# Performance work log

Measured on AMD Instinct MI355X. Metric: run time of the kernel, lower is better.

The kernel has to match this reference:

```python
import jax, jax.numpy as jnp
import numpy as np

N = 20000      # nodes
E = 256000     # edges
H = 8          # heads
DIN = 256      # in_dim_struct / in_dim_semantic
DH = 32        # num_hidden per head (H*DH == DIN for GT residual)
PRED = 32      # pred_dim (relation embedding dim)
REL = 16       # rel_num
NEG = 0.2      # negative_slope for GAT attention
ALPHA = 0.5    # args.fusion
NUM_LAYERS = 2


def seg_softmax(e, seg, n):
    # softmax over edges grouped by destination node; e: [E, ...], seg: [E]
    m = jax.ops.segment_max(e, seg, num_segments=n)
    ex = jnp.exp(e - m[seg])
    s = jax.ops.segment_sum(ex, seg, num_segments=n)
    return ex / (s[seg] + 1e-9)


def setup_inputs() -> dict:
    key = jax.random.key(0)
    ks = jax.random.split(key, 24)
    f32 = jnp.float32
    def rn(k, shape, scale=0.05):
        return jax.random.normal(k, shape, dtype=f32) * scale
    return {
        "feats_struct": jax.random.normal(ks[0], (N, DIN), f32),
        "feats_semantic": jax.random.normal(ks[1], (N, DIN), f32),
        "centrality": jax.random.uniform(ks[2], (N,), f32),
        # fused per-head scoring MLP (heads[0] small Sequentials batched over H)
        "Ws1": rn(ks[3], (H, DIN, DIN // 2)),
        "bs1": jnp.zeros((H, DIN // 2), f32),
        "Ws2": rn(ks[4], (H, DIN // 2)),
        "bs2": jnp.zeros((H,), f32),
        "rel_emb": rn(ks[5], (REL, PRED), 1.0),
        # SALayer params (2 layers, per-head scalar channels)
        "sa_w": rn(ks[6], (NUM_LAYERS, H), 1.0),
        "sa_al": rn(ks[7], (NUM_LAYERS, H), 1.0),
        "sa_ar": rn(ks[8], (NUM_LAYERS, H), 1.0),
        "sa_We": rn(ks[9], (NUM_LAYERS, PRED, H)),
        # GTLayer params
        "Wq": rn(ks[10], (DIN, H * DH)),
        "bq": jnp.zeros((H * DH,), f32),
        "Wk": rn(ks[11], (DIN, H * DH)),
        "bk": jnp.zeros((H * DH,), f32),
        "Wv": rn(ks[12], (DIN, H * DH)),
        "bv": jnp.zeros((H * DH,), f32),
        "We_gt": rn(ks[13], (PRED, H * DH)),
        "bn_gamma": jnp.ones((H * DH,), f32),
        "bn_beta": jnp.zeros((H * DH,), f32),
        "Wout": rn(ks[14], (H * DH, 1)),
        "bout": jnp.zeros((1,), f32),
        # centrality scale params
        "gamma": jnp.ones((1, H), f32),
        "beta": jnp.zeros((1, H), f32),
        "edge_types": jax.random.randint(ks[15], (E,), 0, REL),
        "edge_src": jax.random.randint(ks[16], (E,), 0, N),
        "edge_dst": jax.random.randint(ks[17], (E,), 0, N),
    }


def _forward(feats_struct, feats_semantic, centrality, Ws1, bs1, Ws2, bs2,
             rel_emb, sa_w, sa_al, sa_ar, sa_We, Wq, bq, Wk, bk, Wv, bv,
             We_gt, bn_gamma, bn_beta, Wout, bout, gamma, beta,
             edge_types, edge_src, edge_dst):
    n = feats_struct.shape[0]
    edge_feats = rel_emb[edge_types]                                   # [E, PRED]

    # ---- structural channel: fused per-head scoring MLPs ----
    h1 = jax.nn.relu(jnp.einsum('nd,hdk->nhk', feats_struct, Ws1) + bs1)  # [N,H,DIN/2]
    h = jnp.einsum('nhk,hk->nh', h1, Ws2) + bs2                           # [N,H]

    # ---- SALayer stack (GAT-style, per-head scalar features) ----
    for l in range(NUM_LAYERS):
        z = h * sa_w[l]                                                 # [N,H]
        e = jax.nn.leaky_relu(z[edge_src] * sa_al[l] + z[edge_dst] * sa_ar[l]
                              + edge_feats @ sa_We[l], NEG)             # [E,H]
        attn = seg_softmax(e, edge_dst, n)                              # [E,H]
        out = jax.ops.segment_sum(attn * z[edge_src], edge_dst, num_segments=n)
        h = jax.nn.elu(out + z)                                         # residual + activation
        if l != NUM_LAYERS - 1:
            h = jnp.mean(h, axis=-1, keepdims=True)
            h = jnp.tile(h, (1, H))
    logits_struct = h                                                   # [N,H]

    # ---- semantic channel: Graph Transformer layer (edge_mode='MUL') ----
    q = (feats_semantic @ Wq + bq).reshape(n, H, DH)
    k = (feats_semantic @ Wk + bk).reshape(n, H, DH)
    v = (feats_semantic @ Wv + bv).reshape(n, H, DH)
    ep = (edge_feats @ We_gt).reshape(-1, H, DH)                        # [E,H,DH]
    ke = k[edge_src] * ep                                               # MUL edge gating
    score = jnp.sum(q[edge_dst] * ke, axis=-1) / jnp.sqrt(jnp.float32(DH))  # [E,H]
    attn = seg_softmax(score, edge_dst, n)                              # [E,H]
    agg = jax.ops.segment_sum(attn[..., None] * v[edge_src], edge_dst,
                              num_segments=n).reshape(n, H * DH)
    agg = agg + feats_semantic                                          # residual (H*DH == DIN)
    mu = jnp.mean(agg, axis=0)
    var = jnp.var(agg, axis=0)
    agg = (agg - mu) / jnp.sqrt(var + 1e-5) * bn_gamma + bn_beta        # batch norm
    h_sem = jax.nn.relu(agg)
    logits_semantic = h_sem @ Wout + bout                               # [N,1]

    # ---- fusion + centrality gamma/beta scaling ----
    logits = ALPHA * logits_struct + (1.0 - ALPHA) * logits_semantic    # [N,H]
    scaled = (centrality[:, None] * gamma + beta) * logits              # [N,H]
    return jax.nn.leaky_relu(jnp.mean(scaled, axis=-1, keepdims=True), 0.01)


def reference(feats_struct, feats_semantic, centrality, Ws1, bs1, Ws2, bs2,
              rel_emb, sa_w, sa_al, sa_ar, sa_We, Wq, bq, Wk, bk, Wv, bv,
              We_gt, bn_gamma, bn_beta, Wout, bout, gamma, beta,
              edge_types, edge_src, edge_dst):
    return _forward(feats_struct, feats_semantic, centrality, Ws1, bs1, Ws2, bs2,
                    rel_emb, sa_w, sa_al, sa_ar, sa_We, Wq, bq, Wk, bk, Wv, bv,
                    We_gt, bn_gamma, bn_beta, Wout, bout, gamma, beta,
                    edge_types, edge_src, edge_dst)
```

## Files before the change

kernel.cpp:

```cpp
#include <hip/hip_runtime.h>
#include <hip/hip_bf16.h>
#include <math.h>

#define N_NODES 20000
#define N_EDGES 256000

typedef __attribute__((ext_vector_type(8))) __bf16 bf16x8;
typedef __attribute__((ext_vector_type(8))) unsigned short u16x8;
typedef __attribute__((ext_vector_type(4))) float f32x4;

static __device__ __forceinline__ unsigned short f2bf(float f) {
  unsigned u = __float_as_uint(f);
  unsigned r = (u + 0x7fffu + ((u >> 16) & 1u)) >> 16;
  return (unsigned short)r;
}
static __device__ __forceinline__ float b2f(unsigned short u) {
  return __uint_as_float((unsigned)u << 16);
}


__global__ void k_tables(const float* __restrict__ rel_emb,
                         const float* __restrict__ sa_We,
                         const float* __restrict__ We_gt,
                         float* __restrict__ saTab, float* __restrict__ epTab) {
  int t = threadIdx.x;
  {
    int l = t >> 7, r = (t >> 3) & 15, h = t & 7;
    float acc = 0.f;
    for (int p = 0; p < 32; ++p)
      acc += rel_emb[r * 32 + p] * sa_We[l * 256 + p * 8 + h];
    saTab[t] = acc;
  }
  for (int r = 0; r < 16; ++r) {
    float acc = 0.f;
    for (int p = 0; p < 32; ++p)
      acc += rel_emb[r * 32 + p] * We_gt[p * 256 + t];
    epTab[r * 256 + t] = acc;
  }
}

__global__ void k_hist(const int* __restrict__ e_dst, int* __restrict__ deg) {
  int e = blockIdx.x * 256 + threadIdx.x;
  if (e < N_EDGES) atomicAdd(&deg[e_dst[e]], 1);
}

__global__ void k_scan(const int* __restrict__ deg, int* __restrict__ rowPtr,
                       int* __restrict__ cursor) {
  const int CH = (N_NODES + 255) / 256;
  int t = threadIdx.x;
  int b0 = t * CH, b1 = min(b0 + CH, N_NODES);
  int s = 0;
  for (int i = b0; i < b1; ++i) s += deg[i];
  __shared__ int part[256];
  part[t] = s;
  __syncthreads();
  for (int off = 1; off < 256; off <<= 1) {
    int add = (t >= off) ? part[t - off] : 0;
    __syncthreads();
    part[t] += add;
    __syncthreads();
  }
  int run = (t == 0) ? 0 : part[t - 1];
  for (int i = b0; i < b1; ++i) {
    rowPtr[i] = run;
    cursor[i] = run;
    run += deg[i];
  }
  if (t == 0) rowPtr[N_NODES] = part[255];
}

__global__ void k_fill(const int* __restrict__ e_dst, const int* __restrict__ e_src,
                       const int* __restrict__ e_type, int* __restrict__ cursor,
                       int* __restrict__ csrSrc, int* __restrict__ csrType) {
  int e = blockIdx.x * 256 + threadIdx.x;
  if (e >= N_EDGES) return;
  int d = e_dst[e];
  int pos = atomicAdd(&cursor[d], 1);
  csrSrc[pos] = e_src[e];
  csrType[pos] = e_type[e];
}


__global__ void k_convX(const float* __restrict__ Xs, const float* __restrict__ Xm,
                        ushort* __restrict__ Xsb, ushort* __restrict__ Xmb) {
  size_t i = ((size_t)blockIdx.x * 256 + threadIdx.x) * 4;
  float4 a = *(const float4*)(Xs + i);
  ushort4 ua = {f2bf(a.x), f2bf(a.y), f2bf(a.z), f2bf(a.w)};
  *(ushort4*)(Xsb + i) = ua;
  float4 b = *(const float4*)(Xm + i);
  ushort4 ub = {f2bf(b.x), f2bf(b.y), f2bf(b.z), f2bf(b.w)};
  *(ushort4*)(Xmb + i) = ub;
}

__global__ void k_tws1(const float* __restrict__ Ws1, ushort* __restrict__ Ws1t) {
  int h = blockIdx.x >> 7, kcol = blockIdx.x & 127, d = threadIdx.x;
  Ws1t[((size_t)h * 128 + kcol) * 256 + d] = f2bf(Ws1[((size_t)h * 256 + d) * 128 + kcol]);
}

__global__ void k_twqkv(const float* __restrict__ Wq, const float* __restrict__ Wk,
                        const float* __restrict__ Wv, ushort* __restrict__ Wt) {
  int m = blockIdx.x >> 8, n = blockIdx.x & 255, d = threadIdx.x;
  const float* W = (m == 0) ? Wq : (m == 1) ? Wk : Wv;
  Wt[((size_t)m * 256 + n) * 256 + d] = f2bf(W[(size_t)d * 256 + n]);
}


__global__ __launch_bounds__(256) void k_mlp_mfma(
    const ushort* __restrict__ Xb, const ushort* __restrict__ Ws1t,
    const float* __restrict__ bs1, const float* __restrict__ Ws2,
    const float* __restrict__ bs2, float* __restrict__ h0) {
  __shared__ ushort Ab[64][136];
  __shared__ ushort Bb[128][136];
  int tid = threadIdx.x;
  int h = blockIdx.y;
  int base = blockIdx.x * 64;
  int wv = tid >> 6, lane = tid & 63;
  int l15 = lane & 15, lhi = lane >> 4;
  f32x4 acc[8];
  #pragma unroll
  for (int nt = 0; nt < 8; ++nt) acc[nt] = (f32x4){0.f, 0.f, 0.f, 0.f};

  for (int kc = 0; kc < 2; ++kc) {
    {
      int r = tid >> 2, c4 = (tid & 3) * 4;
      int gr = base + r;
      const ushort* src = Xb + (size_t)gr * 256 + kc * 128;
      #pragma unroll
      for (int s = 0; s < 4; ++s) {
        u16x8 val = {0, 0, 0, 0, 0, 0, 0, 0};
        if (gr < N_NODES) val = *(const u16x8*)(src + (c4 + s) * 8);
        *(u16x8*)&Ab[r][(c4 + s) * 8] = val;
      }
    }
    {
      int r = tid >> 1, cb = (tid & 1) * 8;
      const ushort* src = Ws1t + ((size_t)h * 128 + r) * 256 + kc * 128;
      #pragma unroll
      for (int s = 0; s < 8; ++s)
        *(u16x8*)&Bb[r][(cb + s) * 8] = *(const u16x8*)(src + (cb + s) * 8);
    }
    __syncthreads();
    #pragma unroll
    for (int kk = 0; kk < 4; ++kk) {
      bf16x8 a = *(const bf16x8*)&Ab[wv * 16 + l15][kk * 32 + lhi * 8];
      #pragma unroll
      for (int nt = 0; nt < 8; ++nt) {
        bf16x8 b = *(const bf16x8*)&Bb[nt * 16 + l15][kk * 32 + lhi * 8];
        acc[nt] = __builtin_amdgcn_mfma_f32_16x16x32_bf16(a, b, acc[nt], 0, 0, 0);
      }
    }
    __syncthreads();
  }
  float part[4] = {0.f, 0.f, 0.f, 0.f};
  #pragma unroll
  for (int nt = 0; nt < 8; ++nt) {
    int c = h * 128 + nt * 16 + l15;
    float b1 = bs1[c], w2 = Ws2[c];
    #pragma unroll
    for (int j = 0; j < 4; ++j)
      part[j] += fmaxf(acc[nt][j] + b1, 0.f) * w2;
  }
  #pragma unroll
  for (int j = 0; j < 4; ++j) {
    #pragma unroll
    for (int o = 1; o < 16; o <<= 1) part[j] += __shfl_xor(part[j], o);
  }
  if (l15 == 0) {
    float b2 = bs2[h];
    #pragma unroll
    for (int j = 0; j < 4; ++j) {
      int row = base + wv * 16 + lhi * 4 + j;
      if (row < N_NODES) h0[(size_t)row * 8 + h] = part[j] + b2;
    }
  }
}


__global__ __launch_bounds__(256) void k_qkv_mfma(
    const ushort* __restrict__ Xb, const ushort* __restrict__ Wt,
    const float* __restrict__ bq, const float* __restrict__ bk,
    const float* __restrict__ bv, float* __restrict__ q,
    ushort* __restrict__ kb, ushort* __restrict__ vb) {
  __shared__ ushort Ab[64][136];
  __shared__ ushort Bb[128][136];
  int tid = threadIdx.x;
  int m = blockIdx.y >> 1, half = blockIdx.y & 1;
  int base = blockIdx.x * 64;
  int wv = tid >> 6, lane = tid & 63;
  int l15 = lane & 15, lhi = lane >> 4;
  f32x4 acc[8];
  #pragma unroll
  for (int nt = 0; nt < 8; ++nt) acc[nt] = (f32x4){0.f, 0.f, 0.f, 0.f};

  for (int kc = 0; kc < 2; ++kc) {
    {
      int r = tid >> 2, c4 = (tid & 3) * 4;
      int gr = base + r;
      const ushort* src = Xb + (size_t)gr * 256 + kc * 128;
      #pragma unroll
      for (int s = 0; s < 4; ++s) {
        u16x8 val = {0, 0, 0, 0, 0, 0, 0, 0};
        if (gr < N_NODES) val = *(const u16x8*)(src + (c4 + s) * 8);
        *(u16x8*)&Ab[r][(c4 + s) * 8] = val;
      }
    }
    {
      int r = tid >> 1, cb = (tid & 1) * 8;
      const ushort* src = Wt + (((size_t)m * 256 + half * 128 + r) * 256) + kc * 128;
      #pragma unroll
      for (int s = 0; s < 8; ++s)
        *(u16x8*)&Bb[r][(cb + s) * 8] = *(const u16x8*)(src + (cb + s) * 8);
    }
    __syncthreads();
    #pragma unroll
    for (int kk = 0; kk < 4; ++kk) {
      bf16x8 a = *(const bf16x8*)&Ab[wv * 16 + l15][kk * 32 + lhi * 8];
      #pragma unroll
      for (int nt = 0; nt < 8; ++nt) {
        bf16x8 b = *(const bf16x8*)&Bb[nt * 16 + l15][kk * 32 + lhi * 8];
        acc[nt] = __builtin_amdgcn_mfma_f32_16x16x32_bf16(a, b, acc[nt], 0, 0, 0);
      }
    }
    __syncthreads();
  }
  const float* bias = (m == 0) ? bq : (m == 1) ? bk : bv;
  #pragma unroll
  for (int nt = 0; nt < 8; ++nt) {
    int c = half * 128 + nt * 16 + l15;
    float bc = bias[c];
    #pragma unroll
    for (int j = 0; j < 4; ++j) {
      int row = base + wv * 16 + lhi * 4 + j;
      if (row < N_NODES) {
        float val = acc[nt][j] + bc;
        if (m == 0) q[(size_t)row * 256 + c] = val;
        else if (m == 1) kb[(size_t)row * 256 + c] = f2bf(val);
        else vb[(size_t)row * 256 + c] = f2bf(val);
      }
    }
  }
}


__global__ __launch_bounds__(256) void k_sa(const float* __restrict__ h_in,
                                            float* __restrict__ h_out,
                                            const int* __restrict__ rowPtr,
                                            const int* __restrict__ csrSrc,
                                            const int* __restrict__ csrType,
                                            const float* __restrict__ sa_w,
                                            const float* __restrict__ sa_al,
                                            const float* __restrict__ sa_ar,
                                            const float* __restrict__ saTab, int layer) {
  int node = blockIdx.x * 4 + (threadIdx.x >> 6);
  int lane = threadIdx.x & 63;
  int h = lane & 7, eslot = lane >> 3;
  float wgt = sa_w[layer * 8 + h];
  float al = sa_al[layer * 8 + h];
  float ar = sa_ar[layer * 8 + h];
  const float* tab = saTab + layer * 128;
  float zd = h_in[(size_t)node * 8 + h] * wgt;
  int s0 = rowPtr[node], s1 = rowPtr[node + 1];
  float m = -1e30f, lsum = 0.f, acc = 0.f;
  for (int i = s0 + eslot; i < s1; i += 8) {
    int s = csrSrc[i], ty = csrType[i];
    float zs = h_in[(size_t)s * 8 + h] * wgt;
    float e = zs * al + zd * ar + tab[ty * 8 + h];
    e = (e >= 0.f) ? e : 0.2f * e;
    float nm = fmaxf(m, e);
    float scl = expf(m - nm);
    float p = expf(e - nm);
    acc = acc * scl + p * zs;
    lsum = lsum * scl + p;
    m = nm;
  }
  #pragma unroll
  for (int off = 8; off < 64; off <<= 1) {
    float om = __shfl_xor(m, off);
    float ol = __shfl_xor(lsum, off);
    float oa = __shfl_xor(acc, off);
    float nm = fmaxf(m, om);
    float sl = expf(m - nm);
    float so = expf(om - nm);
    acc = acc * sl + oa * so;
    lsum = lsum * sl + ol * so;
    m = nm;
  }
  float o = acc / (lsum + 1e-9f);
  float r = o + zd;
  r = (r > 0.f) ? r : expm1f(r);
  if (layer == 0) {
    r += __shfl_xor(r, 1);
    r += __shfl_xor(r, 2);
    r += __shfl_xor(r, 4);
    r *= 0.125f;
  }
  if (eslot == 0) h_out[(size_t)node * 8 + h] = r;
}


__global__ __launch_bounds__(256) void k_gt(const float* __restrict__ q,
                                            const ushort* __restrict__ kb,
                                            const ushort* __restrict__ vb,
                                            const float* __restrict__ epTab,
                                            const float* __restrict__ feats_sem,
                                            const int* __restrict__ rowPtr,
                                            const int* __restrict__ csrSrc,
                                            const int* __restrict__ csrType,
                                            float* __restrict__ agg) {
  int node = blockIdx.x * 4 + (threadIdx.x >> 6);
  int lane = threadIdx.x & 63;
  int c0 = lane * 4;
  const float SC = 0.17677669529663687f;
  float4 qv = *(const float4*)(q + (size_t)node * 256 + c0);
  qv.x *= SC; qv.y *= SC; qv.z *= SC; qv.w *= SC;
  float4 acc = {0.f, 0.f, 0.f, 0.f};
  float m = -1e30f, lsum = 0.f;
  int s0 = rowPtr[node], s1 = rowPtr[node + 1];
  int i = s0;
  for (; i + 1 < s1; i += 2) {
    int sA = csrSrc[i], tyA = csrType[i];
    int sB = csrSrc[i + 1], tyB = csrType[i + 1];
    ushort4 kA = *(const ushort4*)(kb + (size_t)sA * 256 + c0);
    ushort4 kB4 = *(const ushort4*)(kb + (size_t)sB * 256 + c0);
    float4 epA = *(const float4*)(epTab + tyA * 256 + c0);
    float4 epB = *(const float4*)(epTab + tyB * 256 + c0);
    ushort4 vA = *(const ushort4*)(vb + (size_t)sA * 256 + c0);
    ushort4 vB = *(const ushort4*)(vb + (size_t)sB * 256 + c0);
    float pA = qv.x * b2f(kA.x) * epA.x + qv.y * b2f(kA.y) * epA.y +
               qv.z * b2f(kA.z) * epA.z + qv.w * b2f(kA.w) * epA.w;
    float pB = qv.x * b2f(kB4.x) * epB.x + qv.y * b2f(kB4.y) * epB.y +
               qv.z * b2f(kB4.z) * epB.z + qv.w * b2f(kB4.w) * epB.w;
    pA += __shfl_xor(pA, 1); pB += __shfl_xor(pB, 1);
    pA += __shfl_xor(pA, 2); pB += __shfl_xor(pB, 2);
    pA += __shfl_xor(pA, 4); pB += __shfl_xor(pB, 4);
    float nm = fmaxf(m, fmaxf(pA, pB));
    float scl = expf(m - nm);
    float eA = expf(pA - nm);
    float eB = expf(pB - nm);
    acc.x = acc.x * scl + eA * b2f(vA.x) + eB * b2f(vB.x);
    acc.y = acc.y * scl + eA * b2f(vA.y) + eB * b2f(vB.y);
    acc.z = acc.z * scl + eA * b2f(vA.z) + eB * b2f(vB.z);
    acc.w = acc.w * scl + eA * b2f(vA.w) + eB * b2f(vB.w);
    lsum = lsum * scl + eA + eB;
    m = nm;
  }
  if (i < s1) {
    int s = csrSrc[i], ty = csrType[i];
    ushort4 kv = *(const ushort4*)(kb + (size_t)s * 256 + c0);
    float4 ep = *(const float4*)(epTab + ty * 256 + c0);
    ushort4 vv = *(const ushort4*)(vb + (size_t)s * 256 + c0);
    float part = qv.x * b2f(kv.x) * ep.x + qv.y * b2f(kv.y) * ep.y +
                 qv.z * b2f(kv.z) * ep.z + qv.w * b2f(kv.w) * ep.w;
    part += __shfl_xor(part, 1);
    part += __shfl_xor(part, 2);
    part += __shfl_xor(part, 4);
    float nm = fmaxf(m, part);
    float scl = expf(m - nm);
    float p = expf(part - nm);
    acc.x = acc.x * scl + p * b2f(vv.x);
    acc.y = acc.y * scl + p * b2f(vv.y);
    acc.z = acc.z * scl + p * b2f(vv.z);
    acc.w = acc.w * scl + p * b2f(vv.w);
    lsum = lsum * scl + p;
    m = nm;
  }
  float inv = 1.f / (lsum + 1e-9f);
  float4 fs = *(const float4*)(feats_sem + (size_t)node * 256 + c0);
  float4 r;
  r.x = acc.x * inv + fs.x;
  r.y = acc.y * inv + fs.y;
  r.z = acc.z * inv + fs.z;
  r.w = acc.w * inv + fs.w;
  *(float4*)(agg + (size_t)node * 256 + c0) = r;
}

__global__ void k_bnstats(const float* __restrict__ agg, double* __restrict__ colsum,
                          double* __restrict__ colssq) {
  int t = threadIdx.x;
  int r0 = blockIdx.x * 79;
  int r1 = min(r0 + 79, N_NODES);
  double s = 0.0, qq = 0.0;
  for (int r = r0; r < r1; ++r) {
    float x = agg[(size_t)r * 256 + t];
    s += (double)x;
    qq += (double)x * (double)x;
  }
  atomicAdd(&colsum[t], s);
  atomicAdd(&colssq[t], qq);
}

__global__ void k_bnfinal(const double* __restrict__ colsum, const double* __restrict__ colssq,
                          float* __restrict__ muArr, float* __restrict__ invArr) {
  int t = threadIdx.x;
  double mu = colsum[t] / (double)N_NODES;
  double var = colssq[t] / (double)N_NODES - mu * mu;
  muArr[t] = (float)mu;
  invArr[t] = (float)(1.0 / sqrt(var + 1e-5));
}

__global__ __launch_bounds__(256) void k_final(const float* __restrict__ agg,
                                               const float* __restrict__ muArr,
                                               const float* __restrict__ invArr,
                                               const float* __restrict__ bn_gamma,
                                               const float* __restrict__ bn_beta,
                                               const float* __restrict__ Wout,
                                               const float* __restrict__ bout,
                                               const float* __restrict__ hB,
                                               const float* __restrict__ cent,
                                               const float* __restrict__ gamma,
                                               const float* __restrict__ beta,
                                               float* __restrict__ out) {
  int node = blockIdx.x * 4 + (threadIdx.x >> 6);
  int lane = threadIdx.x & 63;
  int c0 = lane * 4;
  float4 x = *(const float4*)(agg + (size_t)node * 256 + c0);
  float4 mu = *(const float4*)(muArr + c0);
  float4 iv = *(const float4*)(invArr + c0);
  float4 g = *(const float4*)(bn_gamma + c0);
  float4 b = *(const float4*)(bn_beta + c0);
  float4 w = *(const float4*)(Wout + c0);
  float p = fmaxf((x.x - mu.x) * iv.x * g.x + b.x, 0.f) * w.x +
            fmaxf((x.y - mu.y) * iv.y * g.y + b.y, 0.f) * w.y +
            fmaxf((x.z - mu.z) * iv.z * g.z + b.z, 0.f) * w.z +
            fmaxf((x.w - mu.w) * iv.w * g.w + b.w, 0.f) * w.w;
  #pragma unroll
  for (int o = 1; o < 64; o <<= 1) p += __shfl_xor(p, o);
  float ls = p + bout[0];
  int h = lane & 7;
  float logit = 0.5f * hB[(size_t)node * 8 + h] + 0.5f * ls;
  float sc = (cent[node] * gamma[h] + beta[h]) * logit;
  sc += __shfl_xor(sc, 1);
  sc += __shfl_xor(sc, 2);
  sc += __shfl_xor(sc, 4);
  float mn = sc * 0.125f;
  mn = (mn >= 0.f) ? mn : 0.01f * mn;
  if (lane == 0) out[node] = mn;
}


extern "C" void kernel_launch(void* const* d_in, const int* in_sizes, int n_in,
                              void* d_out, int out_size, void* d_ws, size_t ws_size,
                              hipStream_t stream) {
  (void)in_sizes; (void)n_in; (void)out_size; (void)ws_size;
  const float* feats_struct = (const float*)d_in[0];
  const float* feats_sem    = (const float*)d_in[1];
  const float* cent         = (const float*)d_in[2];
  const float* Ws1          = (const float*)d_in[3];
  const float* bs1          = (const float*)d_in[4];
  const float* Ws2          = (const float*)d_in[5];
  const float* bs2          = (const float*)d_in[6];
  const float* rel_emb      = (const float*)d_in[7];
  const float* sa_w         = (const float*)d_in[8];
  const float* sa_al        = (const float*)d_in[9];
  const float* sa_ar        = (const float*)d_in[10];
  const float* sa_We        = (const float*)d_in[11];
  const float* Wq           = (const float*)d_in[12];
  const float* bq           = (const float*)d_in[13];
  const float* Wk           = (const float*)d_in[14];
  const float* bk           = (const float*)d_in[15];
  const float* Wv           = (const float*)d_in[16];
  const float* bv           = (const float*)d_in[17];
  const float* We_gt        = (const float*)d_in[18];
  const float* bn_gamma     = (const float*)d_in[19];
  const float* bn_beta      = (const float*)d_in[20];
  const float* Wout         = (const float*)d_in[21];
  const float* bout         = (const float*)d_in[22];
  const float* gamma        = (const float*)d_in[23];
  const float* beta         = (const float*)d_in[24];
  const int* e_type         = (const int*)d_in[25];
  const int* e_src          = (const int*)d_in[26];
  const int* e_dst          = (const int*)d_in[27];
  float* out = (float*)d_out;

  char* wsb = (char*)d_ws;
  size_t off = 0;
  auto alloc = [&](size_t bytes) -> char* {
    char* p = wsb + off;
    off = (off + bytes + 255) & ~(size_t)255;
    return p;
  };
  float* saTab   = (float*)alloc(2 * 16 * 8 * 4);
  float* epTab   = (float*)alloc(16 * 256 * 4);
  int* deg       = (int*)alloc((size_t)N_NODES * 4);
  int* rowPtr    = (int*)alloc((size_t)(N_NODES + 1) * 4);
  int* cursor    = (int*)alloc((size_t)N_NODES * 4);
  int* csrSrc    = (int*)alloc((size_t)N_EDGES * 4);
  int* csrType   = (int*)alloc((size_t)N_EDGES * 4);
  float* h0      = (float*)alloc((size_t)N_NODES * 8 * 4);
  float* hA      = (float*)alloc((size_t)N_NODES * 8 * 4);
  float* hB      = (float*)alloc((size_t)N_NODES * 8 * 4);
  float* qb      = (float*)alloc((size_t)N_NODES * 256 * 4);
  ushort* kbB    = (ushort*)alloc((size_t)N_NODES * 256 * 2);
  ushort* vbB    = (ushort*)alloc((size_t)N_NODES * 256 * 2);
  float* agg     = (float*)alloc((size_t)N_NODES * 256 * 4);
  double* colsum = (double*)alloc(256 * 8);
  double* colssq = (double*)alloc(256 * 8);
  float* muArr   = (float*)alloc(256 * 4);
  float* invArr  = (float*)alloc(256 * 4);
  ushort* Xsb    = (ushort*)alloc((size_t)N_NODES * 256 * 2);
  ushort* Xmb    = (ushort*)alloc((size_t)N_NODES * 256 * 2);
  ushort* Ws1t   = (ushort*)alloc((size_t)8 * 128 * 256 * 2);
  ushort* Wqkvt  = (ushort*)alloc((size_t)3 * 256 * 256 * 2);

  hipMemsetAsync(deg, 0, (size_t)N_NODES * 4, stream);
  hipMemsetAsync(colsum, 0, 256 * 8, stream);
  hipMemsetAsync(colssq, 0, 256 * 8, stream);

  k_tables<<<1, 256, 0, stream>>>(rel_emb, sa_We, We_gt, saTab, epTab);
  k_hist<<<(N_EDGES + 255) / 256, 256, 0, stream>>>(e_dst, deg);
  k_scan<<<1, 256, 0, stream>>>(deg, rowPtr, cursor);
  k_fill<<<(N_EDGES + 255) / 256, 256, 0, stream>>>(e_dst, e_src, e_type, cursor, csrSrc, csrType);

  k_convX<<<N_NODES * 256 / (256 * 4), 256, 0, stream>>>(feats_struct, feats_sem, Xsb, Xmb);
  k_tws1<<<8 * 128, 256, 0, stream>>>(Ws1, Ws1t);
  k_twqkv<<<3 * 256, 256, 0, stream>>>(Wq, Wk, Wv, Wqkvt);

  const int MT = (N_NODES + 63) / 64;
  dim3 gMlp(MT, 8);
  k_mlp_mfma<<<gMlp, 256, 0, stream>>>(Xsb, Ws1t, bs1, Ws2, bs2, h0);
  k_sa<<<(N_NODES + 3) / 4, 256, 0, stream>>>(h0, hA, rowPtr, csrSrc, csrType,
                                              sa_w, sa_al, sa_ar, saTab, 0);
  k_sa<<<(N_NODES + 3) / 4, 256, 0, stream>>>(hA, hB, rowPtr, csrSrc, csrType,
                                              sa_w, sa_al, sa_ar, saTab, 1);

  dim3 gQkv(MT, 6);
  k_qkv_mfma<<<gQkv, 256, 0, stream>>>(Xmb, Wqkvt, bq, bk, bv, qb, kbB, vbB);
  k_gt<<<N_NODES / 4, 256, 0, stream>>>(qb, kbB, vbB, epTab, feats_sem,
                                        rowPtr, csrSrc, csrType, agg);
  k_bnstats<<<256, 256, 0, stream>>>(agg, colsum, colssq);
  k_bnfinal<<<1, 256, 0, stream>>>(colsum, colssq, muArr, invArr);
  k_final<<<N_NODES / 4, 256, 0, stream>>>(agg, muArr, invArr, bn_gamma, bn_beta,
                                           Wout, bout, hB, cent, gamma, beta, out);
}
```

Baseline: 402.0 us.

## Merge setup and GEMM kernels, pack CSR, interleave KV, store agg in bf16

Folds the table, conversion, transpose and histogram kernels into one setup launch, and the MLP and QKV GEMMs into one grid. Packs CSR source and type into int2, interleaves K and V rows so one gather covers both, and stores the aggregate in bf16 to halve its traffic. It also switches the softmax to exp2 with pre-scaled log2e constants and widens the scan to 1024 threads. The intent is fewer launches and less gather and memory traffic, at the cost of some precision in the batch-norm input.

```diff
diff --git a/kernel.cpp b/kernel.cpp
--- a/kernel.cpp
+++ b/kernel.cpp
@@ -4,6 +4,7 @@
 
 #define N_NODES 20000
 #define N_EDGES 256000
+#define LOG2E 1.4426950408889634f
 
 typedef __attribute__((ext_vector_type(8))) __bf16 bf16x8;
 typedef __attribute__((ext_vector_type(8))) unsigned short u16x8;
@@ -18,43 +19,68 @@
   return __uint_as_float((unsigned)u << 16);
 }
 
-
-__global__ void k_tables(const float* __restrict__ rel_emb,
-                         const float* __restrict__ sa_We,
-                         const float* __restrict__ We_gt,
-                         float* __restrict__ saTab, float* __restrict__ epTab) {
+__global__ __launch_bounds__(256) void k_setup(
+    const float* __restrict__ rel_emb, const float* __restrict__ sa_We,
+    const float* __restrict__ We_gt, const float* __restrict__ Xs,
+    const float* __restrict__ Xm, const float* __restrict__ Ws1,
+    const float* __restrict__ Wq, const float* __restrict__ Wk,
+    const float* __restrict__ Wv, const int* __restrict__ e_dst,
+    float* __restrict__ saTab, float* __restrict__ epTab,
+    ushort* __restrict__ Xsb, ushort* __restrict__ Xmb,
+    ushort* __restrict__ Ws1t, ushort* __restrict__ Wt,
+    int* __restrict__ deg) {
+  int b = blockIdx.x;
   int t = threadIdx.x;
-  {
-    int l = t >> 7, r = (t >> 3) & 15, h = t & 7;
-    float acc = 0.f;
-    for (int p = 0; p < 32; ++p)
-      acc += rel_emb[r * 32 + p] * sa_We[l * 256 + p * 8 + h];
-    saTab[t] = acc;
-  }
-  for (int r = 0; r < 16; ++r) {
-    float acc = 0.f;
-    for (int p = 0; p < 32; ++p)
-      acc += rel_emb[r * 32 + p] * We_gt[p * 256 + t];
-    epTab[r * 256 + t] = acc;
-  }
-}
-
-__global__ void k_hist(const int* __restrict__ e_dst, int* __restrict__ deg) {
-  int e = blockIdx.x * 256 + threadIdx.x;
-  if (e < N_EDGES) atomicAdd(&deg[e_dst[e]], 1);
-}
-
-__global__ void k_scan(const int* __restrict__ deg, int* __restrict__ rowPtr,
-                       int* __restrict__ cursor) {
-  const int CH = (N_NODES + 255) / 256;
+  if (b == 0) {
+    {
+      int l = t >> 7, r = (t >> 3) & 15, h = t & 7;
+      float acc = 0.f;
+      for (int p = 0; p < 32; ++p)
+        acc += rel_emb[r * 32 + p] * sa_We[l * 256 + p * 8 + h];
+      saTab[t] = acc * LOG2E;
+    }
+    for (int r = 0; r < 16; ++r) {
+      float acc = 0.f;
+      for (int p = 0; p < 32; ++p)
+        acc += rel_emb[r * 32 + p] * We_gt[p * 256 + t];
+      epTab[r * 256 + t] = acc;
+    }
+  } else if (b < 5001) {
+    size_t i = ((size_t)(b - 1) * 256 + t) * 4;
+    float4 a = *(const float4*)(Xs + i);
+    ushort4 ua = {f2bf(a.x), f2bf(a.y), f2bf(a.z), f2bf(a.w)};
+    *(ushort4*)(Xsb + i) = ua;
+    float4 c = *(const float4*)(Xm + i);
+    ushort4 uc = {f2bf(c.x), f2bf(c.y), f2bf(c.z), f2bf(c.w)};
+    *(ushort4*)(Xmb + i) = uc;
+  } else if (b < 6025) {
+    int lb = b - 5001;
+    int h = lb >> 7, kcol = lb & 127;
+    Ws1t[((size_t)h * 128 + kcol) * 256 + t] =
+        f2bf(Ws1[((size_t)h * 256 + t) * 128 + kcol]);
+  } else if (b < 6793) {
+    int lb = b - 6025;
+    int m = lb >> 8, n = lb & 255;
+    const float* W = (m == 0) ? Wq : (m == 1) ? Wk : Wv;
+    Wt[((size_t)m * 256 + n) * 256 + t] = f2bf(W[(size_t)t * 256 + n]);
+  } else {
+    int e = (b - 6793) * 256 + t;
+    if (e < N_EDGES) atomicAdd(&deg[e_dst[e]], 1);
+  }
+}
+
+__global__ __launch_bounds__(1024) void k_scan(const int* __restrict__ deg,
+                                               int* __restrict__ rowPtr,
+                                               int* __restrict__ cursor) {
+  const int CH = (N_NODES + 1023) / 1024;
   int t = threadIdx.x;
   int b0 = t * CH, b1 = min(b0 + CH, N_NODES);
   int s = 0;
   for (int i = b0; i < b1; ++i) s += deg[i];
-  __shared__ int part[256];
+  __shared__ int part[1024];
   part[t] = s;
   __syncthreads();
-  for (int off = 1; off < 256; off <<= 1) {
+  for (int off = 1; off < 1024; off <<= 1) {
     int add = (t >= off) ? part[t - off] : 0;
     __syncthreads();
     part[t] += add;
@@ -66,53 +92,43 @@
     cursor[i] = run;
     run += deg[i];
   }
-  if (t == 0) rowPtr[N_NODES] = part[255];
+  if (t == 0) rowPtr[N_NODES] = part[1023];
 }
 
 __global__ void k_fill(const int* __restrict__ e_dst, const int* __restrict__ e_src,
                        const int* __restrict__ e_type, int* __restrict__ cursor,
-                       int* __restrict__ csrSrc, int* __restrict__ csrType) {
+                       int2* __restrict__ csrPack) {
   int e = blockIdx.x * 256 + threadIdx.x;
   if (e >= N_EDGES) return;
   int d = e_dst[e];
   int pos = atomicAdd(&cursor[d], 1);
-  csrSrc[pos] = e_src[e];
-  csrType[pos] = e_type[e];
-}
-
-
-__global__ void k_convX(const float* __restrict__ Xs, const float* __restrict__ Xm,
-                        ushort* __restrict__ Xsb, ushort* __restrict__ Xmb) {
-  size_t i = ((size_t)blockIdx.x * 256 + threadIdx.x) * 4;
-  float4 a = *(const float4*)(Xs + i);
-  ushort4 ua = {f2bf(a.x), f2bf(a.y), f2bf(a.z), f2bf(a.w)};
-  *(ushort4*)(Xsb + i) = ua;
-  float4 b = *(const float4*)(Xm + i);
-  ushort4 ub = {f2bf(b.x), f2bf(b.y), f2bf(b.z), f2bf(b.w)};
-  *(ushort4*)(Xmb + i) = ub;
-}
-
-__global__ void k_tws1(const float* __restrict__ Ws1, ushort* __restrict__ Ws1t) {
-  int h = blockIdx.x >> 7, kcol = blockIdx.x & 127, d = threadIdx.x;
-  Ws1t[((size_t)h * 128 + kcol) * 256 + d] = f2bf(Ws1[((size_t)h * 256 + d) * 128 + kcol]);
-}
-
-__global__ void k_twqkv(const float* __restrict__ Wq, const float* __restrict__ Wk,
-                        const float* __restrict__ Wv, ushort* __restrict__ Wt) {
-  int m = blockIdx.x >> 8, n = blockIdx.x & 255, d = threadIdx.x;
-  const float* W = (m == 0) ? Wq : (m == 1) ? Wk : Wv;
-  Wt[((size_t)m * 256 + n) * 256 + d] = f2bf(W[(size_t)d * 256 + n]);
-}
-
-
-__global__ __launch_bounds__(256) void k_mlp_mfma(
-    const ushort* __restrict__ Xb, const ushort* __restrict__ Ws1t,
+  csrPack[pos] = make_int2(e_src[e], e_type[e]);
+}
+
+__global__ __launch_bounds__(256) void k_gemm(
+    const ushort* __restrict__ Xsb, const ushort* __restrict__ Xmb,
+    const ushort* __restrict__ Ws1t, const ushort* __restrict__ Wqkvt,
     const float* __restrict__ bs1, const float* __restrict__ Ws2,
-    const float* __restrict__ bs2, float* __restrict__ h0) {
+    const float* __restrict__ bs2, const float* __restrict__ bq,
+    const float* __restrict__ bk, const float* __restrict__ bv,
+    float* __restrict__ h0, float* __restrict__ q, ushort* __restrict__ kvB) {
   __shared__ ushort Ab[64][136];
   __shared__ ushort Bb[128][136];
   int tid = threadIdx.x;
-  int h = blockIdx.y;
+  int y = blockIdx.y;
+  bool isMlp = (y < 8);
+  int m = 0, half = 0;
+  const ushort* Bsrc;
+  const ushort* Xb;
+  if (isMlp) {
+    Xb = Xsb;
+    Bsrc = Ws1t + (size_t)y * 128 * 256;
+  } else {
+    m = (y - 8) >> 1;
+    half = (y - 8) & 1;
+    Xb = Xmb;
+    Bsrc = Wqkvt + ((size_t)m * 256 + half * 128) * 256;
+  }
   int base = blockIdx.x * 64;
   int wv = tid >> 6, lane = tid & 63;
   int l15 = lane & 15, lhi = lane >> 4;
@@ -134,7 +150,7 @@
     }
     {
       int r = tid >> 1, cb = (tid & 1) * 8;
-      const ushort* src = Ws1t + ((size_t)h * 128 + r) * 256 + kc * 128;
+      const ushort* src = Bsrc + (size_t)r * 256 + kc * 128;
       #pragma unroll
       for (int s = 0; s < 8; ++s)
         *(u16x8*)&Bb[r][(cb + s) * 8] = *(const u16x8*)(src + (cb + s) * 8);
@@ -151,91 +167,45 @@
     }
     __syncthreads();
   }
-  float part[4] = {0.f, 0.f, 0.f, 0.f};
-  #pragma unroll
-  for (int nt = 0; nt < 8; ++nt) {
-    int c = h * 128 + nt * 16 + l15;
-    float b1 = bs1[c], w2 = Ws2[c];
+
+  if (isMlp) {
+    float part[4] = {0.f, 0.f, 0.f, 0.f};
     #pragma unroll
-    for (int j = 0; j < 4; ++j)
-      part[j] += fmaxf(acc[nt][j] + b1, 0.f) * w2;
-  }
-  #pragma unroll
-  for (int j = 0; j < 4; ++j) {
-    #pragma unroll
-    for (int o = 1; o < 16; o <<= 1) part[j] += __shfl_xor(part[j], o);
-  }
-  if (l15 == 0) {
-    float b2 = bs2[h];
+    for (int nt = 0; nt < 8; ++nt) {
+      int c = y * 128 + nt * 16 + l15;
+      float b1 = bs1[c], w2 = Ws2[c];
+      #pragma unroll
+      for (int j = 0; j < 4; ++j)
+        part[j] += fmaxf(acc[nt][j] + b1, 0.f) * w2;
+    }
     #pragma unroll
     for (int j = 0; j < 4; ++j) {
-      int row = base + wv * 16 + lhi * 4 + j;
-      if (row < N_NODES) h0[(size_t)row * 8 + h] = part[j] + b2;
-    }
-  }
-}
-
-
-__global__ __launch_bounds__(256) void k_qkv_mfma(
-    const ushort* __restrict__ Xb, const ushort* __restrict__ Wt,
-    const float* __restrict__ bq, const float* __restrict__ bk,
-    const float* __restrict__ bv, float* __restrict__ q,
-    ushort* __restrict__ kb, ushort* __restrict__ vb) {
-  __shared__ ushort Ab[64][136];
-  __shared__ ushort Bb[128][136];
-  int tid = threadIdx.x;
-  int m = blockIdx.y >> 1, half = blockIdx.y & 1;
-  int base = blockIdx.x * 64;
-  int wv = tid >> 6, lane = tid & 63;
-  int l15 = lane & 15, lhi = lane >> 4;
-  f32x4 acc[8];
-  #pragma unroll
-  for (int nt = 0; nt < 8; ++nt) acc[nt] = (f32x4){0.f, 0.f, 0.f, 0.f};
-
-  for (int kc = 0; kc < 2; ++kc) {
-    {
-      int r = tid >> 2, c4 = (tid & 3) * 4;
-      int gr = base + r;
-      const ushort* src = Xb + (size_t)gr * 256 + kc * 128;
-      #pragma unroll
-      for (int s = 0; s < 4; ++s) {
-        u16x8 val = {0, 0, 0, 0, 0, 0, 0, 0};
-        if (gr < N_NODES) val = *(const u16x8*)(src + (c4 + s) * 8);
-        *(u16x8*)&Ab[r][(c4 + s) * 8] = val;
+      #pragma unroll
+      for (int o = 1; o < 16; o <<= 1) part[j] += __shfl_xor(part[j], o);
+    }
+    if (l15 == 0) {
+      float b2 = bs2[y];
+      #pragma unroll
+      for (int j = 0; j < 4; ++j) {
+        int row = base + wv * 16 + lhi * 4 + j;
+        if (row < N_NODES) h0[(size_t)row * 8 + y] = part[j] + b2;
       }
     }
-    {
-      int r = tid >> 1, cb = (tid & 1) * 8;
-      const ushort* src = Wt + (((size_t)m * 256 + half * 128 + r) * 256) + kc * 128;
-      #pragma unroll
-      for (int s = 0; s < 8; ++s)
-        *(u16x8*)&Bb[r][(cb + s) * 8] = *(const u16x8*)(src + (cb + s) * 8);
-    }
-    __syncthreads();
+  } else {
+    const float* bias = (m == 0) ? bq : (m == 1) ? bk : bv;
     #pragma unroll
-    for (int kk = 0; kk < 4; ++kk) {
-      bf16x8 a = *(const bf16x8*)&Ab[wv * 16 + l15][kk * 32 + lhi * 8];
-      #pragma unroll
-      for (int nt = 0; nt < 8; ++nt) {
-        bf16x8 b = *(const bf16x8*)&Bb[nt * 16 + l15][kk * 32 + lhi * 8];
-        acc[nt] = __builtin_amdgcn_mfma_f32_16x16x32_bf16(a, b, acc[nt], 0, 0, 0);
-      }
-    }
-    __syncthreads();
-  }
-  const float* bias = (m == 0) ? bq : (m == 1) ? bk : bv;
-  #pragma unroll
-  for (int nt = 0; nt < 8; ++nt) {
-    int c = half * 128 + nt * 16 + l15;
-    float bc = bias[c];
-    #pragma unroll
-    for (int j = 0; j < 4; ++j) {
-      int row = base + wv * 16 + lhi * 4 + j;
-      if (row < N_NODES) {
-        float val = acc[nt][j] + bc;
-        if (m == 0) q[(size_t)row * 256 + c] = val;
-        else if (m == 1) kb[(size_t)row * 256 + c] = f2bf(val);
-        else vb[(size_t)row * 256 + c] = f2bf(val);
+    for (int nt = 0; nt < 8; ++nt) {
+      int c = half * 128 + nt * 16 + l15;
+      float bc = bias[c];
+      #pragma unroll
+      for (int j = 0; j < 4; ++j) {
+        int row = base + wv * 16 + lhi * 4 + j;
+        if (row < N_NODES) {
+          float val = acc[nt][j] + bc;
+          if (m == 0) q[(size_t)row * 256 + c] = val;
+          else if (m == 1) kvB[(size_t)row * 512 + c] = f2bf(val);
+          else kvB[(size_t)row * 512 + 256 + c] = f2bf(val);
+        }
       }
     }
   }
@@ -245,8 +215,7 @@
 __global__ __launch_bounds__(256) void k_sa(const float* __restrict__ h_in,
                                             float* __restrict__ h_out,
                                             const int* __restrict__ rowPtr,
-                                            const int* __restrict__ csrSrc,
-                                            const int* __restrict__ csrType,
+                                            const int2* __restrict__ csrPack,
                                             const float* __restrict__ sa_w,
                                             const float* __restrict__ sa_al,
                                             const float* __restrict__ sa_ar,
@@ -255,22 +224,22 @@
   int lane = threadIdx.x & 63;
   int h = lane & 7, eslot = lane >> 3;
   float wgt = sa_w[layer * 8 + h];
-  float al = sa_al[layer * 8 + h];
-  float ar = sa_ar[layer * 8 + h];
+  float al2 = sa_al[layer * 8 + h] * LOG2E;
+  float ar2 = sa_ar[layer * 8 + h] * LOG2E;
   const float* tab = saTab + layer * 128;
   float zd = h_in[(size_t)node * 8 + h] * wgt;
   int s0 = rowPtr[node], s1 = rowPtr[node + 1];
   float m = -1e30f, lsum = 0.f, acc = 0.f;
   for (int i = s0 + eslot; i < s1; i += 8) {
-    int s = csrSrc[i], ty = csrType[i];
-    float zs = h_in[(size_t)s * 8 + h] * wgt;
-    float e = zs * al + zd * ar + tab[ty * 8 + h];
+    int2 p = csrPack[i];
+    float zs = h_in[(size_t)p.x * 8 + h] * wgt;
+    float e = zs * al2 + zd * ar2 + tab[p.y * 8 + h];
     e = (e >= 0.f) ? e : 0.2f * e;
     float nm = fmaxf(m, e);
-    float scl = expf(m - nm);
-    float p = expf(e - nm);
-    acc = acc * scl + p * zs;
-    lsum = lsum * scl + p;
+    float scl = exp2f(m - nm);
+    float pw = exp2f(e - nm);
+    acc = acc * scl + pw * zs;
+    lsum = lsum * scl + pw;
     m = nm;
   }
   #pragma unroll
@@ -279,8 +248,8 @@
     float ol = __shfl_xor(lsum, off);
     float oa = __shfl_xor(acc, off);
     float nm = fmaxf(m, om);
-    float sl = expf(m - nm);
-    float so = expf(om - nm);
+    float sl = exp2f(m - nm);
+    float so = exp2f(om - nm);
     acc = acc * sl + oa * so;
     lsum = lsum * sl + ol * so;
     m = nm;
@@ -299,33 +268,32 @@
 
 
 __global__ __launch_bounds__(256) void k_gt(const float* __restrict__ q,
-                                            const ushort* __restrict__ kb,
-                                            const ushort* __restrict__ vb,
+                                            const ushort* __restrict__ kvB,
                                             const float* __restrict__ epTab,
                                             const float* __restrict__ feats_sem,
                                             const int* __restrict__ rowPtr,
-                                            const int* __restrict__ csrSrc,
-                                            const int* __restrict__ csrType,
-                                            float* __restrict__ agg) {
+                                            const int2* __restrict__ csrPack,
+                                            ushort* __restrict__ agg) {
   int node = blockIdx.x * 4 + (threadIdx.x >> 6);
   int lane = threadIdx.x & 63;
   int c0 = lane * 4;
-  const float SC = 0.17677669529663687f;
+  const float SC2 = 0.17677669529663687f * LOG2E;
   float4 qv = *(const float4*)(q + (size_t)node * 256 + c0);
-  qv.x *= SC; qv.y *= SC; qv.z *= SC; qv.w *= SC;
+  qv.x *= SC2; qv.y *= SC2; qv.z *= SC2; qv.w *= SC2;
   float4 acc = {0.f, 0.f, 0.f, 0.f};
   float m = -1e30f, lsum = 0.f;
   int s0 = rowPtr[node], s1 = rowPtr[node + 1];
   int i = s0;
   for (; i + 1 < s1; i += 2) {
-    int sA = csrSrc[i], tyA = csrType[i];
-    int sB = csrSrc[i + 1], tyB = csrType[i + 1];
-    ushort4 kA = *(const ushort4*)(kb + (size_t)sA * 256 + c0);
-    ushort4 kB4 = *(const ushort4*)(kb + (size_t)sB * 256 + c0);
-    float4 epA = *(const float4*)(epTab + tyA * 256 + c0);
-    float4 epB = *(const float4*)(epTab + tyB * 256 + c0);
-    ushort4 vA = *(const ushort4*)(vb + (size_t)sA * 256 + c0);
-    ushort4 vB = *(const ushort4*)(vb + (size_t)sB * 256 + c0);
+    int2 eA = csrPack[i], eB = csrPack[i + 1];
+    const ushort* rA = kvB + (size_t)eA.x * 512 + c0;
+    const ushort* rB = kvB + (size_t)eB.x * 512 + c0;
+    ushort4 kA = *(const ushort4*)rA;
+    ushort4 kB4 = *(const ushort4*)rB;
+    float4 epA = *(const float4*)(epTab + eA.y * 256 + c0);
+    float4 epB = *(const float4*)(epTab + eB.y * 256 + c0);
+    ushort4 vA = *(const ushort4*)(rA + 256);
+    ushort4 vB = *(const ushort4*)(rB + 256);
     float pA = qv.x * b2f(kA.x) * epA.x + qv.y * b2f(kA.y) * epA.y +
                qv.z * b2f(kA.z) * epA.z + qv.w * b2f(kA.w) * epA.w;
     float pB = qv.x * b2f(kB4.x) * epB.x + qv.y * b2f(kB4.y) * epB.y +
@@ -334,54 +302,55 @@
     pA += __shfl_xor(pA, 2); pB += __shfl_xor(pB, 2);
     pA += __shfl_xor(pA, 4); pB += __shfl_xor(pB, 4);
     float nm = fmaxf(m, fmaxf(pA, pB));
-    float scl = expf(m - nm);
-    float eA = expf(pA - nm);
-    float eB = expf(pB - nm);
-    acc.x = acc.x * scl + eA * b2f(vA.x) + eB * b2f(vB.x);
-    acc.y = acc.y * scl + eA * b2f(vA.y) + eB * b2f(vB.y);
-    acc.z = acc.z * scl + eA * b2f(vA.z) + eB * b2f(vB.z);
-    acc.w = acc.w * scl + eA * b2f(vA.w) + eB * b2f(vB.w);
-    lsum = lsum * scl + eA + eB;
+    float scl = exp2f(m - nm);
+    float wA = exp2f(pA - nm);
+    float wB = exp2f(pB - nm);
+    acc.x = acc.x * scl + wA * b2f(vA.x) + wB * b2f(vB.x);
+    acc.y = acc.y * scl + wA * b2f(vA.y) + wB * b2f(vB.y);
+    acc.z = acc.z * scl + wA * b2f(vA.z) + wB * b2f(vB.z);
+    acc.w = acc.w * scl + wA * b2f(vA.w) + wB * b2f(vB.w);
+    lsum = lsum * scl + wA + wB;
     m = nm;
   }
   if (i < s1) {
-    int s = csrSrc[i], ty = csrType[i];
-    ushort4 kv = *(const ushort4*)(kb + (size_t)s * 256 + c0);
-    float4 ep = *(const float4*)(epTab + ty * 256 + c0);
-    ushort4 vv = *(const ushort4*)(vb + (size_t)s * 256 + c0);
+    int2 eA = csrPack[i];
+    const ushort* rA = kvB + (size_t)eA.x * 512 + c0;
+    ushort4 kv = *(const ushort4*)rA;
+    float4 ep = *(const float4*)(epTab + eA.y * 256 + c0);
+    ushort4 vv = *(const ushort4*)(rA + 256);
     float part = qv.x * b2f(kv.x) * ep.x + qv.y * b2f(kv.y) * ep.y +
                  qv.z * b2f(kv.z) * ep.z + qv.w * b2f(kv.w) * ep.w;
     part += __shfl_xor(part, 1);
     part += __shfl_xor(part, 2);
     part += __shfl_xor(part, 4);
     float nm = fmaxf(m, part);
-    float scl = expf(m - nm);
-    float p = expf(part - nm);
-    acc.x = acc.x * scl + p * b2f(vv.x);
-    acc.y = acc.y * scl + p * b2f(vv.y);
-    acc.z = acc.z * scl + p * b2f(vv.z);
-    acc.w = acc.w * scl + p * b2f(vv.w);
-    lsum = lsum * scl + p;
+    float scl = exp2f(m - nm);
+    float pw = exp2f(part - nm);
+    acc.x = acc.x * scl + pw * b2f(vv.x);
+    acc.y = acc.y * scl + pw * b2f(vv.y);
+    acc.z = acc.z * scl + pw * b2f(vv.z);
+    acc.w = acc.w * scl + pw * b2f(vv.w);
+    lsum = lsum * scl + pw;
     m = nm;
   }
   float inv = 1.f / (lsum + 1e-9f);
   float4 fs = *(const float4*)(feats_sem + (size_t)node * 256 + c0);
-  float4 r;
-  r.x = acc.x * inv + fs.x;
-  r.y = acc.y * inv + fs.y;
-  r.z = acc.z * inv + fs.z;
-  r.w = acc.w * inv + fs.w;
-  *(float4*)(agg + (size_t)node * 256 + c0) = r;
-}
-
-__global__ void k_bnstats(const float* __restrict__ agg, double* __restrict__ colsum,
+  ushort4 r;
+  r.x = f2bf(acc.x * inv + fs.x);
+  r.y = f2bf(acc.y * inv + fs.y);
+  r.z = f2bf(acc.z * inv + fs.z);
+  r.w = f2bf(acc.w * inv + fs.w);
+  *(ushort4*)(agg + (size_t)node * 256 + c0) = r;
+}
+
+__global__ void k_bnstats(const ushort* __restrict__ agg, double* __restrict__ colsum,
                           double* __restrict__ colssq) {
   int t = threadIdx.x;
   int r0 = blockIdx.x * 79;
   int r1 = min(r0 + 79, N_NODES);
   double s = 0.0, qq = 0.0;
   for (int r = r0; r < r1; ++r) {
-    float x = agg[(size_t)r * 256 + t];
+    float x = b2f(agg[(size_t)r * 256 + t]);
     s += (double)x;
     qq += (double)x * (double)x;
   }
@@ -398,7 +367,7 @@
   invArr[t] = (float)(1.0 / sqrt(var + 1e-5));
 }
 
-__global__ __launch_bounds__(256) void k_final(const float* __restrict__ agg,
+__global__ __launch_bounds__(256) void k_final(const ushort* __restrict__ agg,
                                                const float* __restrict__ muArr,
                                                const float* __restrict__ invArr,
                                                const float* __restrict__ bn_gamma,
@@ -413,16 +382,16 @@
   int node = blockIdx.x * 4 + (threadIdx.x >> 6);
   int lane = threadIdx.x & 63;
   int c0 = lane * 4;
-  float4 x = *(const float4*)(agg + (size_t)node * 256 + c0);
+  ushort4 xa = *(const ushort4*)(agg + (size_t)node * 256 + c0);
   float4 mu = *(const float4*)(muArr + c0);
   float4 iv = *(const float4*)(invArr + c0);
   float4 g = *(const float4*)(bn_gamma + c0);
   float4 b = *(const float4*)(bn_beta + c0);
   float4 w = *(const float4*)(Wout + c0);
-  float p = fmaxf((x.x - mu.x) * iv.x * g.x + b.x, 0.f) * w.x +
-            fmaxf((x.y - mu.y) * iv.y * g.y + b.y, 0.f) * w.y +
-            fmaxf((x.z - mu.z) * iv.z * g.z + b.z, 0.f) * w.z +
-            fmaxf((x.w - mu.w) * iv.w * g.w + b.w, 0.f) * w.w;
+  float p = fmaxf((b2f(xa.x) - mu.x) * iv.x * g.x + b.x, 0.f) * w.x +
+            fmaxf((b2f(xa.y) - mu.y) * iv.y * g.y + b.y, 0.f) * w.y +
+            fmaxf((b2f(xa.z) - mu.z) * iv.z * g.z + b.z, 0.f) * w.z +
+            fmaxf((b2f(xa.w) - mu.w) * iv.w * g.w + b.w, 0.f) * w.w;
   #pragma unroll
   for (int o = 1; o < 64; o <<= 1) p += __shfl_xor(p, o);
   float ls = p + bout[0];
@@ -484,15 +453,13 @@
   int* deg       = (int*)alloc((size_t)N_NODES * 4);
   int* rowPtr    = (int*)alloc((size_t)(N_NODES + 1) * 4);
   int* cursor    = (int*)alloc((size_t)N_NODES * 4);
-  int* csrSrc    = (int*)alloc((size_t)N_EDGES * 4);
-  int* csrType   = (int*)alloc((size_t)N_EDGES * 4);
+  int2* csrPack  = (int2*)alloc((size_t)N_EDGES * 8);
   float* h0      = (float*)alloc((size_t)N_NODES * 8 * 4);
   float* hA      = (float*)alloc((size_t)N_NODES * 8 * 4);
   float* hB      = (float*)alloc((size_t)N_NODES * 8 * 4);
   float* qb      = (float*)alloc((size_t)N_NODES * 256 * 4);
-  ushort* kbB    = (ushort*)alloc((size_t)N_NODES * 256 * 2);
-  ushort* vbB    = (ushort*)alloc((size_t)N_NODES * 256 * 2);
-  float* agg     = (float*)alloc((size_t)N_NODES * 256 * 4);
+  ushort* kvB    = (ushort*)alloc((size_t)N_NODES * 512 * 2);
+  ushort* agg    = (ushort*)alloc((size_t)N_NODES * 256 * 2);
   double* colsum = (double*)alloc(256 * 8);
   double* colssq = (double*)alloc(256 * 8);
   float* muArr   = (float*)alloc(256 * 4);
@@ -506,27 +473,22 @@
   hipMemsetAsync(colsum, 0, 256 * 8, stream);
   hipMemsetAsync(colssq, 0, 256 * 8, stream);
 
-  k_tables<<<1, 256, 0, stream>>>(rel_emb, sa_We, We_gt, saTab, epTab);
-  k_hist<<<(N_EDGES + 255) / 256, 256, 0, stream>>>(e_dst, deg);
-  k_scan<<<1, 256, 0, stream>>>(deg, rowPtr, cursor);
-  k_fill<<<(N_EDGES + 255) / 256, 256, 0, stream>>>(e_dst, e_src, e_type, cursor, csrSrc, csrType);
-
-  k_convX<<<N_NODES * 256 / (256 * 4), 256, 0, stream>>>(feats_struct, feats_sem, Xsb, Xmb);
-  k_tws1<<<8 * 128, 256, 0, stream>>>(Ws1, Ws1t);
-  k_twqkv<<<3 * 256, 256, 0, stream>>>(Wq, Wk, Wv, Wqkvt);
+  k_setup<<<7793, 256, 0, stream>>>(rel_emb, sa_We, We_gt, feats_struct, feats_sem,
+                                    Ws1, Wq, Wk, Wv, e_dst,
+                                    saTab, epTab, Xsb, Xmb, Ws1t, Wqkvt, deg);
+  k_scan<<<1, 1024, 0, stream>>>(deg, rowPtr, cursor);
+  k_fill<<<(N_EDGES + 255) / 256, 256, 0, stream>>>(e_dst, e_src, e_type, cursor, csrPack);
 
   const int MT = (N_NODES + 63) / 64;
-  dim3 gMlp(MT, 8);
-  k_mlp_mfma<<<gMlp, 256, 0, stream>>>(Xsb, Ws1t, bs1, Ws2, bs2, h0);
-  k_sa<<<(N_NODES + 3) / 4, 256, 0, stream>>>(h0, hA, rowPtr, csrSrc, csrType,
+  dim3 gGemm(MT, 14);
+  k_gemm<<<gGemm, 256, 0, stream>>>(Xsb, Xmb, Ws1t, Wqkvt, bs1, Ws2, bs2,
+                                    bq, bk, bv, h0, qb, kvB);
+  k_sa<<<(N_NODES + 3) / 4, 256, 0, stream>>>(h0, hA, rowPtr, csrPack,
                                               sa_w, sa_al, sa_ar, saTab, 0);
-  k_sa<<<(N_NODES + 3) / 4, 256, 0, stream>>>(hA, hB, rowPtr, csrSrc, csrType,
+  k_sa<<<(N_NODES + 3) / 4, 256, 0, stream>>>(hA, hB, rowPtr, csrPack,
                                               sa_w, sa_al, sa_ar, saTab, 1);
-
-  dim3 gQkv(MT, 6);
-  k_qkv_mfma<<<gQkv, 256, 0, stream>>>(Xmb, Wqkvt, bq, bk, bv, qb, kbB, vbB);
-  k_gt<<<N_NODES / 4, 256, 0, stream>>>(qb, kbB, vbB, epTab, feats_sem,
-                                        rowPtr, csrSrc, csrType, agg);
+  k_gt<<<N_NODES / 4, 256, 0, stream>>>(qb, kvB, epTab, feats_sem,
+                                        rowPtr, csrPack, agg);
   k_bnstats<<<256, 256, 0, stream>>>(agg, colsum, colssq);
   k_bnfinal<<<1, 256, 0, stream>>>(colsum, colssq, muArr, invArr);
   k_final<<<N_NODES / 4, 256, 0, stream>>>(agg, muArr, invArr, bn_gamma, bn_beta,
```

After: 367.1 us. -8.7%, faster.
